# Kernel tuning notes

Hardware: AMD Instinct MI355X
Metric: run time of the kernel (lower is better)

## Reference

```python
import jax, jax.numpy as jnp
import numpy as np

BS, D_IN, D_H, D_Z = 4096, 784, 400, 20


def setup_inputs() -> dict:
    key = jax.random.key(0)
    ks = jax.random.split(key, 13)
    s = 0.05
    return {
        "x": jax.random.normal(ks[0], (BS, D_IN), dtype=jnp.float32),
        "W1": jax.random.normal(ks[1], (D_H, D_IN), dtype=jnp.float32) * s,
        "b1": jax.random.normal(ks[2], (D_H,), dtype=jnp.float32) * s,
        "W21": jax.random.normal(ks[3], (D_Z, D_H), dtype=jnp.float32) * s,
        "b21": jax.random.normal(ks[4], (D_Z,), dtype=jnp.float32) * s,
        "W22": jax.random.normal(ks[5], (D_Z, D_H), dtype=jnp.float32) * s,
        "b22": jax.random.normal(ks[6], (D_Z,), dtype=jnp.float32) * s,
        "W3": jax.random.normal(ks[7], (D_H, D_Z), dtype=jnp.float32) * s,
        "b3": jax.random.normal(ks[8], (D_H,), dtype=jnp.float32) * s,
        "W41": jax.random.normal(ks[9], (D_IN, D_H), dtype=jnp.float32) * s,
        "b41": jax.random.normal(ks[10], (D_IN,), dtype=jnp.float32) * s,
        "W42": jax.random.normal(ks[11], (D_IN, D_H), dtype=jnp.float32) * s,
        "b42": jax.random.normal(ks[12], (D_IN,), dtype=jnp.float32) * s,
    }


def reference(x, W1, b1, W21, b21, W22, b22, W3, b3, W41, b41, W42, b42):
    xr = x.reshape(-1, D_IN)                              # [bs, 784]
    # encode
    h1 = jax.nn.relu(xr @ W1.T + b1)                      # [bs, 400]
    mu = h1 @ W21.T + b21                                 # [bs, 20]
    logvar = h1 @ W22.T + b22                             # [bs, 20]
    # unscented sigma points: varsqrt[:, i] = sqrt(N)*logvar[:, i]*e_i
    N = D_Z
    sqrtN = jnp.asarray(np.sqrt(N), dtype=x.dtype)
    # delta[i, b, j] = sqrt(N) * logvar[b, i] * (i == j)   -> [N, bs, N]
    delta = sqrtN * logvar.T[:, :, None] * jnp.eye(N, dtype=x.dtype)[:, None, :]
    z = jnp.concatenate([mu[None] + delta, mu[None] - delta], axis=0)  # [2N, bs, N]

    def decode(zs):
        h3 = jax.nn.relu(zs @ W3.T + b3)                  # [bs, 400]
        return zs @ W41.T * 0 + (h3 @ W41.T + b41), h3 @ W42.T + b42

    def decode_clean(zs):
        h3 = jax.nn.relu(zs @ W3.T + b3)
        return h3 @ W41.T + b41, h3 @ W42.T + b42

    # original loop decodes every sigma point; recon_x keeps the last one
    mu_x, var_x = jax.vmap(decode_clean)(z)               # each [2N, bs, 784]
    recon_mu = mu_x[-1]
    recon_var = var_x[-1]
    return recon_mu, recon_var, mu, logvar, z
```

## Files before the change

### kernel.cpp

```cpp
#include <hip/hip_runtime.h>
#include <hip/hip_bf16.h>

#define BS   4096
#define DIN  784
#define DH   400
#define DZ   20

#define KP1  832
#define KPH  416
#define KPD  448

#define OFF_RMU  0
#define OFF_RVAR 3211264
#define OFF_MU   6422528
#define OFF_LV   6504448
#define OFF_Z    6586368

#define WS_WCAT  0
#define WS_W2C   1404928
#define WS_W1B   1444864
#define WS_H1B   2110464
#define WS_H3B   5518336

#define SQRT20F 4.47213595499958f

using short8 = __attribute__((ext_vector_type(8))) short;
using f4     = __attribute__((ext_vector_type(4))) float;
using i4     = __attribute__((ext_vector_type(4))) int;

__device__ __forceinline__ short bf16r(float f) {
    union { float f; unsigned u; } v; v.f = f;
    unsigned r = (v.u + 0x7fffu + ((v.u >> 16) & 1u)) >> 16;
    return (short)r;
}

__device__ __forceinline__ void glds16(const void* g, void* l) {
    __builtin_amdgcn_global_load_lds(
        (const __attribute__((address_space(1))) unsigned int*)g,
        (__attribute__((address_space(3))) unsigned int*)l,
        16, 0, 0);
}

__global__ void k0(const float* __restrict__ W1, const float* __restrict__ W41,
                   const float* __restrict__ W42, const float* __restrict__ W21,
                   const float* __restrict__ W22, char* __restrict__ ws) {
    const int N0 = 400 * 104;
    const int N1 = N0 + 1568 * 56;
    const int N2 = N1 + 48 * 52;
    int gid = blockIdx.x * 256 + threadIdx.x;
    if (gid >= N2) return;

    const float* sr = nullptr;
    short* dst;
    int c, DC;
    if (gid < N0) {
        int row = gid / 104; c = gid - row * 104; DC = 98;
        sr = W1 + (size_t)row * DIN;
        dst = (short*)(ws + WS_W1B) + (size_t)row * KP1 + c * 8;
    } else if (gid < N1) {
        int p = gid - N0;
        int row = p / 56; c = p - row * 56; DC = 50;
        sr = (row < 784) ? (W41 + (size_t)row * DH) : (W42 + (size_t)(row - 784) * DH);
        dst = (short*)(ws + WS_WCAT) + (size_t)row * KPD + c * 8;
    } else {
        int p = gid - N1;
        int row = p / 52; c = p - row * 52; DC = 50;
        if (row < 20)      sr = W21 + (size_t)row * DH;
        else if (row < 40) sr = W22 + (size_t)(row - 20) * DH;
        else               sr = nullptr;
        dst = (short*)(ws + WS_W2C) + (size_t)row * KPH + c * 8;
    }
    short8 v;
    if (c < DC && sr) {
        f4 a = *(const f4*)(sr + c * 8);
        f4 b = *(const f4*)(sr + c * 8 + 4);
#pragma unroll
        for (int e = 0; e < 4; ++e) { v[e] = bf16r(a[e]); v[4 + e] = bf16r(b[e]); }
    } else {
#pragma unroll
        for (int e = 0; e < 8; ++e) v[e] = 0;
    }
    *(short8*)dst = v;
}

__global__ __launch_bounds__(256)
void k1(const float* __restrict__ x, const float* __restrict__ b1,
        const short* __restrict__ W1b, short* __restrict__ h1b) {
    __shared__ short sA[2][64 * 64];
    __shared__ short sB[2][80 * 64];

    const int tid = threadIdx.x;
    const int bid = blockIdx.x;
    const int swz = (bid & 7) * 40 + (bid >> 3);
    const int bm = swz / 5, bn = swz - bm * 5;
    const int w = tid >> 6, l = tid & 63, lg = l >> 4, lr = l & 15;

    f4 acc[5] = {};
    i4 ar[4];

    auto a_load = [&](int kt) {
#pragma unroll
        for (int i = 0; i < 2; ++i) {
            int c = tid + i * 256;
            int row = c >> 3, kc = c & 7;
            int gk = kt * 64 + kc * 8;
            if (gk < DIN) {
                const int* src = (const int*)(x + (size_t)(bm * 64 + row) * DIN + gk);
                ar[2 * i] = *(const i4*)src;
                ar[2 * i + 1] = *(const i4*)(src + 4);
            } else {
                ar[2 * i] = (i4){0, 0, 0, 0};
                ar[2 * i + 1] = (i4){0, 0, 0, 0};
            }
        }
    };
    auto a_write = [&](int buf) {
#pragma unroll
        for (int i = 0; i < 2; ++i) {
            int c = tid + i * 256;
            int row = c >> 3, kc = c & 7;
            short8 v;
#pragma unroll
            for (int e = 0; e < 4; ++e) {
                v[e]     = (short)(((unsigned)ar[2 * i][e]) >> 16);
                v[4 + e] = (short)(((unsigned)ar[2 * i + 1][e]) >> 16);
            }
            *(short8*)&sA[buf][(row * 8 + (kc ^ (row & 7))) * 8] = v;
        }
    };
    auto b_stage = [&](int buf, int kt) {
#pragma unroll
        for (int it = 0; it < 3; ++it) {
            int p = it * 256 + tid;
            if (p < 640) {
                int r = p >> 3, kc = (p & 7) ^ (r & 7);
                glds16(W1b + (size_t)(bn * 80 + r) * KP1 + kt * 64 + kc * 8, &sB[buf][p * 8]);
            }
        }
    };
    auto compute = [&](int buf) {
        const int row = w * 16 + lr;
#pragma unroll
        for (int kk = 0; kk < 2; ++kk) {
            short8 a = *(const short8*)&sA[buf][(row * 8 + ((kk * 4 + lg) ^ (row & 7))) * 8];
#pragma unroll
            for (int ni = 0; ni < 5; ++ni) {
                int brw = ni * 16 + lr;
                short8 b = *(const short8*)&sB[buf][(brw * 8 + ((kk * 4 + lg) ^ (brw & 7))) * 8];
                acc[ni] = __builtin_amdgcn_mfma_f32_16x16x32_bf16(a, b, acc[ni], 0, 0, 0);
            }
        }
    };

    a_load(0); b_stage(0, 0); a_write(0);
    __syncthreads();
    for (int kt = 0; kt < 13; ++kt) {
        const int cur = kt & 1;
        if (kt < 12) { a_load(kt + 1); b_stage(cur ^ 1, kt + 1); }
        compute(cur);
        if (kt < 12) a_write(cur ^ 1);
        __syncthreads();
    }

#pragma unroll
    for (int ni = 0; ni < 5; ++ni) {
        int col = bn * 80 + ni * 16 + lr;
        float bias = b1[col];
#pragma unroll
        for (int r = 0; r < 4; ++r) {
            int row = bm * 64 + w * 16 + lg * 4 + r;
            float v = acc[ni][r] + bias;
            h1b[(size_t)row * KPH + col] = bf16r(v > 0.f ? v : 0.f);
        }
    }
    if (bn == 4) {
        for (int p = tid; p < 64 * 16; p += 256) {
            int r = p >> 4, c = 400 + (p & 15);
            h1b[(size_t)(bm * 64 + r) * KPH + c] = 0;
        }
    }
}

__global__ __launch_bounds__(256)
void k_mid(const short* __restrict__ h1b, const short* __restrict__ w2c,
           const float* __restrict__ W3, const float* __restrict__ b3,
           const float* __restrict__ b21, const float* __restrict__ b22,
           float* __restrict__ out, short* __restrict__ h3b) {
    __shared__ short sA[16 * 416];
    __shared__ short sB[48 * 416];
    __shared__ short sW[400 * 40];
    __shared__ float muv[2][16][20];
    __shared__ short zl[16 * 40];
    __shared__ short h3s[16 * 448];

    const int tid = threadIdx.x;
    const int blk = blockIdx.x;
    const int w = tid >> 6, l = tid & 63, lg = l >> 4, lr = l & 15;
    const int r0 = blk * 16;

#pragma unroll
    for (int it = 0; it < 4; ++it) {
        int p = it * 256 + tid;
        if (p < 832) {
            int r = p / 52, cp = p - r * 52, c = cp ^ (r & 3);
            glds16(h1b + (size_t)(r0 + r) * KPH + c * 8, &sA[p * 8]);
        }
    }
#pragma unroll
    for (int it = 0; it < 10; ++it) {
        int p = it * 256 + tid;
        if (p < 2496) {
            int r = p / 52, cp = p - r * 52, c = cp ^ (r & 3);
            glds16(w2c + (size_t)r * KPH + c * 8, &sB[p * 8]);
        }
    }
    if (tid < 200) {
#pragma unroll
        for (int i = 0; i < 2; ++i) {
            int r = tid + i * 200;
            const float* src = W3 + (size_t)r * DZ;
            f4 f0 = *(const f4*)src;
            f4 f1 = *(const f4*)(src + 4);
            f4 f2 = *(const f4*)(src + 8);
            f4 f3 = *(const f4*)(src + 12);
            f4 f5 = *(const f4*)(src + 16);
            short8 c0, c1, c2, c3;
#pragma unroll
            for (int e = 0; e < 4; ++e) {
                c0[e] = bf16r(f0[e]); c0[4 + e] = bf16r(f1[e]);
                c1[e] = bf16r(f2[e]); c1[4 + e] = bf16r(f3[e]);
                c2[e] = bf16r(f5[e]); c2[4 + e] = 0;
                c3[e] = 0; c3[4 + e] = 0;
            }
            *(short8*)&sW[r * 40 + 0]  = c0;
            *(short8*)&sW[r * 40 + 8]  = c1;
            *(short8*)&sW[r * 40 + 16] = c2;
            *(short8*)&sW[r * 40 + 24] = c3;
        }
    }
    __syncthreads();

    if (w == 0) {
        f4 a3[3] = {};
#pragma unroll
        for (int kk = 0; kk < 13; ++kk) {
            short8 a = *(const short8*)&sA[(lr * 52 + ((kk * 4 + lg) ^ (lr & 3))) * 8];
#pragma unroll
            for (int ni = 0; ni < 3; ++ni) {
                int br = ni * 16 + lr;
                short8 b = *(const short8*)&sB[(br * 52 + ((kk * 4 + lg) ^ (br & 3))) * 8];
                a3[ni] = __builtin_amdgcn_mfma_f32_16x16x32_bf16(a, b, a3[ni], 0, 0, 0);
            }
        }
#pragma unroll
        for (int ni = 0; ni < 3; ++ni) {
            int n = ni * 16 + lr;
            if (n < 40) {
                float bias = (n < 20) ? b21[n] : b22[n - 20];
#pragma unroll
                for (int r = 0; r < 4; ++r) {
                    int row = lg * 4 + r;
                    float v = a3[ni][r] + bias;
                    if (n < 20) {
                        muv[0][row][n] = v;
                        out[OFF_MU + (size_t)(r0 + row) * 20 + n] = v;
                    } else {
                        muv[1][row][n - 20] = v;
                        out[OFF_LV + (size_t)(r0 + row) * 20 + (n - 20)] = v;
                    }
                }
            }
        }
    }
    __syncthreads();

    if (tid < 80) {
        int row = tid / 5, c = tid - (tid / 5) * 5;
        short8 v;
#pragma unroll
        for (int e = 0; e < 8; ++e) {
            int j = c * 8 + e;
            float val = 0.f;
            if (j < 20) {
                val = muv[0][row][j];
                if (j == 19) val -= SQRT20F * muv[1][row][19];
            }
            v[e] = bf16r(val);
        }
        *(short8*)&zl[row * 40 + c * 8] = v;
    } else if (tid < 176) {
        int t = tid - 80;
        int row = t / 6, c = t - (t / 6) * 6;
        short8 zz;
#pragma unroll
        for (int e = 0; e < 8; ++e) zz[e] = 0;
        *(short8*)&h3s[row * 448 + 400 + c * 8] = zz;
    }
#pragma unroll
    for (int it = 0; it < 13; ++it) {
        int p = it * 256 + tid;
        if (p < 3200) {
            int s = p / 80, q = p - s * 80;
            int row = q / 5, j4 = q - (q / 5) * 5;
            f4 v = *(const f4*)&muv[0][row][j4 * 4];
            int sp = (s < 20) ? s : s - 20;
            if ((sp >> 2) == j4) {
                float add = ((s < 20) ? SQRT20F : -SQRT20F) * muv[1][row][sp];
                int e = sp & 3;
#pragma unroll
                for (int k = 0; k < 4; ++k) v[k] += (e == k) ? add : 0.f;
            }
            *(f4*)(out + OFF_Z + ((size_t)s * BS + r0 + row) * 20 + j4 * 4) = v;
        }
    }
    __syncthreads();

    for (int f = w; f < 25; f += 4) {
        int n0 = f * 16;
        short8 a = *(const short8*)&zl[lr * 40 + lg * 8];
        short8 b = *(const short8*)&sW[(n0 + lr) * 40 + lg * 8];
        f4 z4 = {};
        f4 accv = __builtin_amdgcn_mfma_f32_16x16x32_bf16(a, b, z4, 0, 0, 0);
        int n = n0 + lr;
        float bias = b3[n];
#pragma unroll
        for (int r = 0; r < 4; ++r) {
            int row = lg * 4 + r;
            float v = accv[r] + bias;
            h3s[row * 448 + n] = bf16r(v > 0.f ? v : 0.f);
        }
    }
    __syncthreads();

#pragma unroll
    for (int it = 0; it < 4; ++it) {
        int p = it * 256 + tid;
        if (p < 896) {
            int row = p / 56, c = p - (p / 56) * 56;
            *(short8*)(h3b + (size_t)(r0 + row) * KPD + c * 8) =
                *(const short8*)&h3s[row * 448 + c * 8];
        }
    }
}

__global__ __launch_bounds__(256)
void k_gemm4(const short* __restrict__ h3b, const short* __restrict__ wcat,
             const float* __restrict__ b41, const float* __restrict__ b42,
             float* __restrict__ out) {
    __shared__ short sA[2][128 * 64];
    __shared__ short sB[2][112 * 64];

    const int tid = threadIdx.x;
    const int bid = blockIdx.x;
    const int swz = (bid & 7) * 56 + (bid >> 3);
    const int bm = swz / 14, bn = swz - bm * 14;
    const int w = tid >> 6, l = tid & 63, lg = l >> 4, lr = l & 15;

    f4 acc[2][7] = {};

    auto stage = [&](int buf, int kt) {
#pragma unroll
        for (int i = 0; i < 4; ++i) {
            int c = tid + i * 256;
            int r = c >> 3, kc = (c & 7) ^ (r & 7);
            glds16(h3b + (size_t)(bm * 128 + r) * KPD + kt * 64 + kc * 8, &sA[buf][c * 8]);
        }
#pragma unroll
        for (int i = 0; i < 4; ++i) {
            int c = tid + i * 256;
            if (c < 896) {
                int r = c >> 3, kc = (c & 7) ^ (r & 7);
                glds16(wcat + (size_t)(bn * 112 + r) * KPD + kt * 64 + kc * 8, &sB[buf][c * 8]);
            }
        }
    };

    stage(0, 0);
    __syncthreads();
    for (int kt = 0; kt < 7; ++kt) {
        const int cur = kt & 1;
        if (kt < 6) stage(cur ^ 1, kt + 1);
        const int row0 = w * 32 + lr, row1 = w * 32 + 16 + lr;
#pragma unroll
        for (int kk = 0; kk < 2; ++kk) {
            short8 a0 = *(const short8*)&sA[cur][(row0 * 8 + ((kk * 4 + lg) ^ (row0 & 7))) * 8];
            short8 a1 = *(const short8*)&sA[cur][(row1 * 8 + ((kk * 4 + lg) ^ (row1 & 7))) * 8];
#pragma unroll
            for (int ni = 0; ni < 7; ++ni) {
                int br = ni * 16 + lr;
                short8 b = *(const short8*)&sB[cur][(br * 8 + ((kk * 4 + lg) ^ (br & 7))) * 8];
                acc[0][ni] = __builtin_amdgcn_mfma_f32_16x16x32_bf16(a0, b, acc[0][ni], 0, 0, 0);
                acc[1][ni] = __builtin_amdgcn_mfma_f32_16x16x32_bf16(a1, b, acc[1][ni], 0, 0, 0);
            }
        }
        __syncthreads();
    }

    const bool first = (bn < 7);
#pragma unroll
    for (int mi = 0; mi < 2; ++mi)
#pragma unroll
        for (int ni = 0; ni < 7; ++ni) {
            int colt = bn * 112 + ni * 16 + lr;
            int cc = first ? colt : colt - 784;
            float bias = first ? b41[cc] : b42[cc];
            size_t base = first ? (size_t)OFF_RMU : (size_t)OFF_RVAR;
#pragma unroll
            for (int r = 0; r < 4; ++r) {
                size_t row = (size_t)(bm * 128 + w * 32 + mi * 16 + lg * 4 + r);
                out[base + row * DIN + cc] = acc[mi][ni][r] + bias;
            }
        }
}

extern "C" void kernel_launch(void* const* d_in, const int* in_sizes, int n_in,
                              void* d_out, int out_size, void* d_ws, size_t ws_size,
                              hipStream_t stream) {
    const float* x   = (const float*)d_in[0];
    const float* W1  = (const float*)d_in[1];
    const float* b1  = (const float*)d_in[2];
    const float* W21 = (const float*)d_in[3];
    const float* b21 = (const float*)d_in[4];
    const float* W22 = (const float*)d_in[5];
    const float* b22 = (const float*)d_in[6];
    const float* W3  = (const float*)d_in[7];
    const float* b3  = (const float*)d_in[8];
    const float* W41 = (const float*)d_in[9];
    const float* b41 = (const float*)d_in[10];
    const float* W42 = (const float*)d_in[11];
    const float* b42 = (const float*)d_in[12];

    float* out = (float*)d_out;
    char*  ws  = (char*)d_ws;
    const short* wcat = (const short*)(ws + WS_WCAT);
    const short* w2c  = (const short*)(ws + WS_W2C);
    const short* W1b  = (const short*)(ws + WS_W1B);
    short* h1b = (short*)(ws + WS_H1B);
    short* h3b = (short*)(ws + WS_H3B);

    k0<<<516, 256, 0, stream>>>(W1, W41, W42, W21, W22, ws);
    k1<<<320, 256, 0, stream>>>(x, b1, W1b, h1b);
    k_mid<<<256, 256, 0, stream>>>(h1b, w2c, W3, b3, b21, b22, out, h3b);
    k_gemm4<<<448, 256, 0, stream>>>(h3b, wcat, b41, b42, out);
}
```

Baseline: 44.98 us.

## Use fine-grained vmcnt waits in GEMM loops and move z-write into gemm4 blocks

The GEMM main loops in k1 and k_gemm4 now use explicit s_waitcnt vmcnt counts and raw s_barrier instead of __syncthreads. This lets the next tile's global-to-LDS loads stay in flight while the current tile is computed. Load slots are reassigned per wave so each wave knows how many outstanding loads it has. The sigma-point z output write moves out of k_mid into 64 extra blocks of k_gemm4, which read mu/logvar back from the output buffer. The bf16 packing in k1's A path is also simplified. The risks are a wrong vmcnt count, which would let compute read LDS before its data arrives, and the extra global reads of mu/logvar in the new z blocks.

After: 54.01 us. 1.2x slower.

```diff
diff --git a/kernel.cpp b/kernel.cpp
--- a/kernel.cpp
+++ b/kernel.cpp
@@ -28,10 +28,25 @@
 using f4     = __attribute__((ext_vector_type(4))) float;
 using i4     = __attribute__((ext_vector_type(4))) int;
 
+#define WAITV(N) asm volatile("s_waitcnt vmcnt(" #N ")" ::: "memory")
+#define WAITL()  asm volatile("s_waitcnt lgkmcnt(0)" ::: "memory")
+#define SBAR()   do { __builtin_amdgcn_sched_barrier(0); \
+                      __builtin_amdgcn_s_barrier();      \
+                      __builtin_amdgcn_sched_barrier(0); } while (0)
+
 __device__ __forceinline__ short bf16r(float f) {
     union { float f; unsigned u; } v; v.f = f;
     unsigned r = (v.u + 0x7fffu + ((v.u >> 16) & 1u)) >> 16;
     return (short)r;
+}
+
+__device__ __forceinline__ i4 pack8(const i4 q0, const i4 q1) {
+    i4 d;
+    d[0] = (q0[1] & 0xffff0000) | (int)(((unsigned)q0[0]) >> 16);
+    d[1] = (q0[3] & 0xffff0000) | (int)(((unsigned)q0[2]) >> 16);
+    d[2] = (q1[1] & 0xffff0000) | (int)(((unsigned)q1[0]) >> 16);
+    d[3] = (q1[3] & 0xffff0000) | (int)(((unsigned)q1[2]) >> 16);
+    return d;
 }
 
 __device__ __forceinline__ void glds16(const void* g, void* l) {
@@ -105,12 +120,10 @@
             int row = c >> 3, kc = c & 7;
             int gk = kt * 64 + kc * 8;
             if (gk < DIN) {
-                const int* src = (const int*)(x + (size_t)(bm * 64 + row) * DIN + gk);
-                ar[2 * i] = *(const i4*)src;
-                ar[2 * i + 1] = *(const i4*)(src + 4);
+                const i4* p = (const i4*)(x + (size_t)(bm * 64 + row) * DIN + gk);
+                ar[2 * i] = p[0]; ar[2 * i + 1] = p[1];
             } else {
-                ar[2 * i] = (i4){0, 0, 0, 0};
-                ar[2 * i + 1] = (i4){0, 0, 0, 0};
+                ar[2 * i] = (i4){0, 0, 0, 0}; ar[2 * i + 1] = (i4){0, 0, 0, 0};
             }
         }
     };
@@ -119,24 +132,18 @@
         for (int i = 0; i < 2; ++i) {
             int c = tid + i * 256;
             int row = c >> 3, kc = c & 7;
-            short8 v;
-#pragma unroll
-            for (int e = 0; e < 4; ++e) {
-                v[e]     = (short)(((unsigned)ar[2 * i][e]) >> 16);
-                v[4 + e] = (short)(((unsigned)ar[2 * i + 1][e]) >> 16);
-            }
-            *(short8*)&sA[buf][(row * 8 + (kc ^ (row & 7))) * 8] = v;
+            *(i4*)&sA[buf][(row * 8 + (kc ^ (row & 7))) * 8] = pack8(ar[2 * i], ar[2 * i + 1]);
         }
     };
     auto b_stage = [&](int buf, int kt) {
-#pragma unroll
-        for (int it = 0; it < 3; ++it) {
-            int p = it * 256 + tid;
-            if (p < 640) {
-                int r = p >> 3, kc = (p & 7) ^ (r & 7);
-                glds16(W1b + (size_t)(bn * 80 + r) * KP1 + kt * 64 + kc * 8, &sB[buf][p * 8]);
-            }
-        }
+        auto one = [&](int slot) {
+            int chunk = slot * 64 + l;
+            int r = chunk >> 3, kc = (chunk & 7) ^ (r & 7);
+            glds16(W1b + (size_t)(bn * 80 + r) * KP1 + kt * 64 + kc * 8,
+                   &sB[buf][chunk * 8]);
+        };
+        one(w); one(4 + w);
+        if (w < 2) one(8 + w);
     };
     auto compute = [&](int buf) {
         const int row = w * 16 + lr;
@@ -153,13 +160,21 @@
     };
 
     a_load(0); b_stage(0, 0); a_write(0);
-    __syncthreads();
+    WAITL();
+
     for (int kt = 0; kt < 13; ++kt) {
         const int cur = kt & 1;
-        if (kt < 12) { a_load(kt + 1); b_stage(cur ^ 1, kt + 1); }
+        if (kt < 12) {
+            a_load(kt + 1); b_stage(cur ^ 1, kt + 1);
+            if (w < 2) WAITV(7); else WAITV(6);
+        } else {
+            WAITV(0);
+        }
+        SBAR();
         compute(cur);
         if (kt < 12) a_write(cur ^ 1);
-        __syncthreads();
+        WAITL();
+        SBAR();
     }
 
 #pragma unroll
@@ -296,23 +311,6 @@
         for (int e = 0; e < 8; ++e) zz[e] = 0;
         *(short8*)&h3s[row * 448 + 400 + c * 8] = zz;
     }
-#pragma unroll
-    for (int it = 0; it < 13; ++it) {
-        int p = it * 256 + tid;
-        if (p < 3200) {
-            int s = p / 80, q = p - s * 80;
-            int row = q / 5, j4 = q - (q / 5) * 5;
-            f4 v = *(const f4*)&muv[0][row][j4 * 4];
-            int sp = (s < 20) ? s : s - 20;
-            if ((sp >> 2) == j4) {
-                float add = ((s < 20) ? SQRT20F : -SQRT20F) * muv[1][row][sp];
-                int e = sp & 3;
-#pragma unroll
-                for (int k = 0; k < 4; ++k) v[k] += (e == k) ? add : 0.f;
-            }
-            *(f4*)(out + OFF_Z + ((size_t)s * BS + r0 + row) * 20 + j4 * 4) = v;
-        }
-    }
     __syncthreads();
 
     for (int f = w; f < 25; f += 4) {
@@ -352,6 +350,28 @@
 
     const int tid = threadIdx.x;
     const int bid = blockIdx.x;
+
+    if (bid >= 448) {
+        const int zb = bid - 448;
+#pragma unroll 2
+        for (int it = 0; it < 50; ++it) {
+            int idx = it * 16384 + zb * 256 + tid;
+            int s = idx / 20480;
+            int rem = idx - s * 20480;
+            int b = rem / 5, j4 = rem - b * 5;
+            int sp = (s < 20) ? s : s - 20;
+            f4 v = *(const f4*)(out + OFF_MU + (size_t)b * 20 + j4 * 4);
+            if ((sp >> 2) == j4) {
+                float add = ((s < 20) ? SQRT20F : -SQRT20F) * out[OFF_LV + (size_t)b * 20 + sp];
+                int e = sp & 3;
+#pragma unroll
+                for (int k = 0; k < 4; ++k) v[k] += (e == k) ? add : 0.f;
+            }
+            *(f4*)(out + OFF_Z + (size_t)idx * 4) = v;
+        }
+        return;
+    }
+
     const int swz = (bid & 7) * 56 + (bid >> 3);
     const int bm = swz / 14, bn = swz - bm * 14;
     const int w = tid >> 6, l = tid & 63, lg = l >> 4, lr = l & 15;
@@ -359,27 +379,33 @@
     f4 acc[2][7] = {};
 
     auto stage = [&](int buf, int kt) {
-#pragma unroll
-        for (int i = 0; i < 4; ++i) {
-            int c = tid + i * 256;
-            int r = c >> 3, kc = (c & 7) ^ (r & 7);
-            glds16(h3b + (size_t)(bm * 128 + r) * KPD + kt * 64 + kc * 8, &sA[buf][c * 8]);
-        }
-#pragma unroll
-        for (int i = 0; i < 4; ++i) {
-            int c = tid + i * 256;
-            if (c < 896) {
-                int r = c >> 3, kc = (c & 7) ^ (r & 7);
-                glds16(wcat + (size_t)(bn * 112 + r) * KPD + kt * 64 + kc * 8, &sB[buf][c * 8]);
-            }
-        }
+        auto oneA = [&](int slot) {
+            int chunk = slot * 64 + l;
+            int r = chunk >> 3, kc = (chunk & 7) ^ (r & 7);
+            glds16(h3b + (size_t)(bm * 128 + r) * KPD + kt * 64 + kc * 8,
+                   &sA[buf][chunk * 8]);
+        };
+        auto oneB = [&](int slot) {
+            int chunk = slot * 64 + l;
+            int r = chunk >> 3, kc = (chunk & 7) ^ (r & 7);
+            glds16(wcat + (size_t)(bn * 112 + r) * KPD + kt * 64 + kc * 8,
+                   &sB[buf][chunk * 8]);
+        };
+        oneA(w); oneA(4 + w); oneA(8 + w); oneA(12 + w);
+        oneB(w); oneB(4 + w); oneB(8 + w);
+        if (w < 2) oneB(12 + w);
     };
 
     stage(0, 0);
-    __syncthreads();
     for (int kt = 0; kt < 7; ++kt) {
         const int cur = kt & 1;
-        if (kt < 6) stage(cur ^ 1, kt + 1);
+        if (kt < 6) {
+            stage(cur ^ 1, kt + 1);
+            if (w < 2) WAITV(8); else WAITV(7);
+        } else {
+            WAITV(0);
+        }
+        SBAR();
         const int row0 = w * 32 + lr, row1 = w * 32 + 16 + lr;
 #pragma unroll
         for (int kk = 0; kk < 2; ++kk) {
@@ -393,7 +419,8 @@
                 acc[1][ni] = __builtin_amdgcn_mfma_f32_16x16x32_bf16(a1, b, acc[1][ni], 0, 0, 0);
             }
         }
-        __syncthreads();
+        WAITL();
+        SBAR();
     }
 
     const bool first = (bn < 7);
@@ -441,5 +468,5 @@
     k0<<<516, 256, 0, stream>>>(W1, W41, W42, W21, W22, ws);
     k1<<<320, 256, 0, stream>>>(x, b1, W1b, h1b);
     k_mid<<<256, 256, 0, stream>>>(h1b, w2c, W3, b3, b21, b22, out, h3b);
-    k_gemm4<<<448, 256, 0, stream>>>(h3b, wcat, b41, b42, out);
-}
+    k_gemm4<<<512, 256, 0, stream>>>(h3b, wcat, b41, b42, out);
+}
```

## Move sigma-point z output writes from k_mid into extra k_gemm4 blocks

Applied to the files above, without the earlier changes.

The large z output write (40 sigma points × 4096 × 20 floats) is removed from k_mid and handled by 64 extra blocks appended to the k_gemm4 grid. Those blocks read mu and logvar back from the output buffer and write z, overlapping this store-heavy work with the decoder GEMM. Separately, the fp32-to-bf16 truncation packing in k1 is rewritten as dword mask/shift ops instead of per-short extraction. The extra blocks compete with the GEMM blocks for CUs and bandwidth.

Result: slower. 51.78 us (+15.1%).

```diff
diff --git a/kernel.cpp b/kernel.cpp
--- a/kernel.cpp
+++ b/kernel.cpp
@@ -32,6 +32,15 @@
     union { float f; unsigned u; } v; v.f = f;
     unsigned r = (v.u + 0x7fffu + ((v.u >> 16) & 1u)) >> 16;
     return (short)r;
+}
+
+__device__ __forceinline__ i4 pack8(const i4 q0, const i4 q1) {
+    i4 d;
+    d[0] = (q0[1] & 0xffff0000) | (int)(((unsigned)q0[0]) >> 16);
+    d[1] = (q0[3] & 0xffff0000) | (int)(((unsigned)q0[2]) >> 16);
+    d[2] = (q1[1] & 0xffff0000) | (int)(((unsigned)q1[0]) >> 16);
+    d[3] = (q1[3] & 0xffff0000) | (int)(((unsigned)q1[2]) >> 16);
+    return d;
 }
 
 __device__ __forceinline__ void glds16(const void* g, void* l) {
@@ -105,12 +114,10 @@
             int row = c >> 3, kc = c & 7;
             int gk = kt * 64 + kc * 8;
             if (gk < DIN) {
-                const int* src = (const int*)(x + (size_t)(bm * 64 + row) * DIN + gk);
-                ar[2 * i] = *(const i4*)src;
-                ar[2 * i + 1] = *(const i4*)(src + 4);
+                const i4* p = (const i4*)(x + (size_t)(bm * 64 + row) * DIN + gk);
+                ar[2 * i] = p[0]; ar[2 * i + 1] = p[1];
             } else {
-                ar[2 * i] = (i4){0, 0, 0, 0};
-                ar[2 * i + 1] = (i4){0, 0, 0, 0};
+                ar[2 * i] = (i4){0, 0, 0, 0}; ar[2 * i + 1] = (i4){0, 0, 0, 0};
             }
         }
     };
@@ -119,13 +126,7 @@
         for (int i = 0; i < 2; ++i) {
             int c = tid + i * 256;
             int row = c >> 3, kc = c & 7;
-            short8 v;
-#pragma unroll
-            for (int e = 0; e < 4; ++e) {
-                v[e]     = (short)(((unsigned)ar[2 * i][e]) >> 16);
-                v[4 + e] = (short)(((unsigned)ar[2 * i + 1][e]) >> 16);
-            }
-            *(short8*)&sA[buf][(row * 8 + (kc ^ (row & 7))) * 8] = v;
+            *(i4*)&sA[buf][(row * 8 + (kc ^ (row & 7))) * 8] = pack8(ar[2 * i], ar[2 * i + 1]);
         }
     };
     auto b_stage = [&](int buf, int kt) {
@@ -296,23 +297,6 @@
         for (int e = 0; e < 8; ++e) zz[e] = 0;
         *(short8*)&h3s[row * 448 + 400 + c * 8] = zz;
     }
-#pragma unroll
-    for (int it = 0; it < 13; ++it) {
-        int p = it * 256 + tid;
-        if (p < 3200) {
-            int s = p / 80, q = p - s * 80;
-            int row = q / 5, j4 = q - (q / 5) * 5;
-            f4 v = *(const f4*)&muv[0][row][j4 * 4];
-            int sp = (s < 20) ? s : s - 20;
-            if ((sp >> 2) == j4) {
-                float add = ((s < 20) ? SQRT20F : -SQRT20F) * muv[1][row][sp];
-                int e = sp & 3;
-#pragma unroll
-                for (int k = 0; k < 4; ++k) v[k] += (e == k) ? add : 0.f;
-            }
-            *(f4*)(out + OFF_Z + ((size_t)s * BS + r0 + row) * 20 + j4 * 4) = v;
-        }
-    }
     __syncthreads();
 
     for (int f = w; f < 25; f += 4) {
@@ -352,6 +336,28 @@
 
     const int tid = threadIdx.x;
     const int bid = blockIdx.x;
+
+    if (bid >= 448) {
+        const int zb = bid - 448;
+#pragma unroll 2
+        for (int it = 0; it < 50; ++it) {
+            int idx = it * 16384 + zb * 256 + tid;
+            int s = idx / 20480;
+            int rem = idx - s * 20480;
+            int b = rem / 5, j4 = rem - b * 5;
+            int sp = (s < 20) ? s : s - 20;
+            f4 v = *(const f4*)(out + OFF_MU + (size_t)b * 20 + j4 * 4);
+            if ((sp >> 2) == j4) {
+                float add = ((s < 20) ? SQRT20F : -SQRT20F) * out[OFF_LV + (size_t)b * 20 + sp];
+                int e = sp & 3;
+#pragma unroll
+                for (int k = 0; k < 4; ++k) v[k] += (e == k) ? add : 0.f;
+            }
+            *(f4*)(out + OFF_Z + (size_t)idx * 4) = v;
+        }
+        return;
+    }
+
     const int swz = (bid & 7) * 56 + (bid >> 3);
     const int bm = swz / 14, bn = swz - bm * 14;
     const int w = tid >> 6, l = tid & 63, lg = l >> 4, lr = l & 15;
@@ -441,5 +447,5 @@
     k0<<<516, 256, 0, stream>>>(W1, W41, W42, W21, W22, ws);
     k1<<<320, 256, 0, stream>>>(x, b1, W1b, h1b);
     k_mid<<<256, 256, 0, stream>>>(h1b, w2c, W3, b3, b21, b22, out, h3b);
-    k_gemm4<<<448, 256, 0, stream>>>(h3b, wcat, b41, b42, out);
-}
+    k_gemm4<<<512, 256, 0, stream>>>(h3b, wcat, b41, b42, out);
+}
```
